# Optimization experiments

Measured on AMD Instinct MI355X. Metric: run time of the kernel, lower is better.

Reference implementation:

```python
import jax, jax.numpy as jnp
import numpy as np

B, T, C = 4, 2048, 1024


def setup_inputs() -> dict:
    key = jax.random.key(0)
    ks = jax.random.split(key, 7)
    s = 1.0 / np.sqrt(C)
    return {
        "x": jax.random.normal(ks[0], (B, T, C), dtype=jnp.float32),
        "Wq": jax.random.normal(ks[1], (C, C), dtype=jnp.float32) * s,
        "bq": jnp.zeros((C,), dtype=jnp.float32),
        "Wk": jax.random.normal(ks[2], (C, C), dtype=jnp.float32) * s,
        "bk": jnp.zeros((C,), dtype=jnp.float32),
        "Wv": jax.random.normal(ks[3], (C, C), dtype=jnp.float32) * s,
        "bv": jnp.zeros((C,), dtype=jnp.float32),
    }


def reference(x, Wq, bq, Wk, bk, Wv, bv):
    # q/k/v projections (torch Linear: x @ W^T + b; here W stored as [C_in, C_out])
    q = x @ Wq + bq  # (B, T, C)
    k = x @ Wk + bk
    v = x @ Wv + bv
    scale = 1.0 / jnp.sqrt(jnp.asarray(C, dtype=x.dtype))
    att = jnp.einsum("btc,bsc->bts", q, k) * scale  # (B, T, T)
    # causal mask: additive -inf above the diagonal
    causal = jnp.tril(jnp.ones((T, T), dtype=bool))
    att = jnp.where(causal, att, jnp.asarray(-jnp.inf, dtype=att.dtype))
    att = jax.nn.softmax(att, axis=-1)
    # dropout is identity in eval/reference mode
    out = jnp.einsum("bts,bsc->btc", att, v)  # (B, T, C)
    return out
```

## Files before the change

### kernel.cpp

```cpp
#include <hip/hip_runtime.h>

#define B_ 4
#define T_ 2048
#define C_ 1024

typedef unsigned short u16;
typedef unsigned int u32;
typedef short sh8 __attribute__((ext_vector_type(8)));
typedef float f32x4 __attribute__((ext_vector_type(4)));

__device__ __forceinline__ float bf2f(u16 u) {
    union { float f; u32 i; } c; c.i = ((u32)u) << 16; return c.f;
}
__device__ __forceinline__ u16 f2bf(float f) {
    union { float f; u32 i; } c; c.f = f;
    return (u16)((c.i + 0x7FFFu + ((c.i >> 16) & 1u)) >> 16);
}

__device__ __forceinline__ void gload_lds16(const void* g, void* l) {
    __builtin_amdgcn_global_load_lds(
        (const __attribute__((address_space(1))) u32*)g,
        (__attribute__((address_space(3))) u32*)l, 16, 0, 0);
}

template<bool RS>
__device__ __forceinline__ void mm_core(
    const u16* __restrict__ A, const u16* __restrict__ B,
    int ldA, int ldB, int nk64,
    u16* lA, u16* lB, f32x4 (&acc)[4][4], f32x4* rsacc, int tid)
{
    const int w  = tid >> 6, l = tid & 63;
    const int fr = l & 15,  fq = l >> 4;
    const int wm = (w & 1) << 6, wn = (w >> 1) << 6;
    const int rl = l >> 3;
    const int pc = l & 7;
    const int cg = pc ^ rl;

    sh8 ones;
    if (RS) {
#pragma unroll
        for (int e = 0; e < 8; ++e) ones[e] = (short)0x3F80;
    }

    for (int kt = 0; kt < nk64; ++kt) {
        const int ko = kt << 6;
#pragma unroll
        for (int t = 0; t < 4; ++t) {
            const int r0 = w * 32 + t * 8;
            const int r  = r0 + rl;
            gload_lds16(A + (size_t)r * ldA + ko + cg * 8, lA + ((size_t)r0 * 8 + l) * 8);
            gload_lds16(B + (size_t)r * ldB + ko + cg * 8, lB + ((size_t)r0 * 8 + l) * 8);
        }
        __syncthreads();
#pragma unroll
        for (int kk = 0; kk < 2; ++kk) {
            sh8 af[4], bf[4];
            const int g = kk * 4 + fq;
#pragma unroll
            for (int i = 0; i < 4; ++i) {
                const int m = wm + i * 16 + fr;
                af[i] = *(const sh8*)(lA + ((size_t)m * 8 + (g ^ (m & 7))) * 8);
                const int n = wn + i * 16 + fr;
                bf[i] = *(const sh8*)(lB + ((size_t)n * 8 + (g ^ (n & 7))) * 8);
            }
#pragma unroll
            for (int i = 0; i < 4; ++i) {
#pragma unroll
                for (int j = 0; j < 4; ++j)
                    acc[i][j] = __builtin_amdgcn_mfma_f32_16x16x32_bf16(af[i], bf[j], acc[i][j], 0, 0, 0);
                if (RS)
                    rsacc[i] = __builtin_amdgcn_mfma_f32_16x16x32_bf16(af[i], ones, rsacc[i], 0, 0, 0);
            }
        }
        __syncthreads();
    }
}

__global__ __launch_bounds__(256) void cvt_all(
    const float* __restrict__ x,
    const float* __restrict__ Wq, const float* __restrict__ Wk, const float* __restrict__ Wv,
    u16* __restrict__ xb, u16* __restrict__ wt)
{
    __shared__ float tile[64][68];
    const int bid = blockIdx.x;
    if (bid < 8192) {
        size_t i = ((size_t)bid * 256 + threadIdx.x) * 4;
        float4 f = *(const float4*)(x + i);
        ushort4 o;
        o.x = f2bf(f.x); o.y = f2bf(f.y); o.z = f2bf(f.z); o.w = f2bf(f.w);
        *(ushort4*)(xb + i) = o;
        return;
    }
    const int r = bid - 8192;
    const int z = r >> 8;
    const int rr = r & 255;
    const int n0 = (rr & 15) * 64, k0 = (rr >> 4) * 64;
    const float* W = z == 0 ? Wq : (z == 1 ? Wk : Wv);
    u16* out = wt + (size_t)z * C_ * C_;
    const int tx = threadIdx.x & 15, ty = threadIdx.x >> 4;
#pragma unroll
    for (int rr2 = 0; rr2 < 4; ++rr2) {
        int row = ty + rr2 * 16;
        *(float4*)&tile[row][tx * 4] = *(const float4*)(W + (size_t)(k0 + row) * C_ + n0 + tx * 4);
    }
    __syncthreads();
#pragma unroll
    for (int rr2 = 0; rr2 < 4; ++rr2) {
        int n = ty + rr2 * 16;
        ushort4 o;
        o.x = f2bf(tile[tx * 4 + 0][n]);
        o.y = f2bf(tile[tx * 4 + 1][n]);
        o.z = f2bf(tile[tx * 4 + 2][n]);
        o.w = f2bf(tile[tx * 4 + 3][n]);
        *(ushort4*)(out + (size_t)(n0 + n) * C_ + k0 + tx * 4) = o;
    }
}

__global__ __launch_bounds__(256, 4) void qkv_mfma(
    const u16* __restrict__ xb, const u16* __restrict__ wt,
    const float* __restrict__ bq, const float* __restrict__ bk, const float* __restrict__ bv,
    u16* __restrict__ qo, u16* __restrict__ ko, u16* __restrict__ vto)
{
    __shared__ __align__(16) u16 smem[17408];
    u16* lA = smem; u16* lB = smem + 8192;
    const int z = blockIdx.z;
    const u16* W = wt + (size_t)z * C_ * C_;
    const float* bias = z == 0 ? bq : (z == 1 ? bk : bv);
    const int n0 = blockIdx.x * 128, m0 = blockIdx.y * 128;
    const int tid = threadIdx.x;
    f32x4 acc[4][4];
#pragma unroll
    for (int i = 0; i < 4; ++i)
#pragma unroll
        for (int j = 0; j < 4; ++j) acc[i][j] = 0.0f;

    mm_core<false>(xb + (size_t)m0 * C_, W + (size_t)n0 * C_, C_, C_, C_ / 64, lA, lB, acc, nullptr, tid);

    const int w = tid >> 6, l = tid & 63, fr = l & 15, fq = l >> 4;
    const int wm = (w & 1) << 6, wn = (w >> 1) << 6;
    if (z < 2) {
#pragma unroll
        for (int i = 0; i < 4; ++i)
#pragma unroll
            for (int j = 0; j < 4; ++j) {
                const int ln = wn + j * 16 + fr;
                const float bb = bias[n0 + ln];
#pragma unroll
                for (int r = 0; r < 4; ++r) {
                    const int lm = wm + i * 16 + fq * 4 + r;
                    smem[lm * 136 + ln] = f2bf(acc[i][j][r] + bb);
                }
            }
        __syncthreads();
        u16* out = z == 0 ? qo : ko;
        const int rr = tid >> 4, cc = tid & 15;
#pragma unroll
        for (int p = 0; p < 8; ++p) {
            const int row = p * 16 + rr;
            uint4 val = *(const uint4*)&smem[row * 136 + cc * 8];
            *(uint4*)(out + (size_t)(m0 + row) * C_ + n0 + cc * 8) = val;
        }
    } else {
#pragma unroll
        for (int i = 0; i < 4; ++i)
#pragma unroll
            for (int j = 0; j < 4; ++j) {
                const int ln = wn + j * 16 + fr;
                const float bb = bias[n0 + ln];
#pragma unroll
                for (int r = 0; r < 4; ++r) {
                    const int lm = wm + i * 16 + fq * 4 + r;
                    smem[lm * 129 + ln] = f2bf(acc[i][j][r] + bb);
                }
            }
        __syncthreads();
        const int b = m0 >> 11;
        const int t0 = m0 & 2047;
        u16* vt = vto + (size_t)b * C_ * T_;
#pragma unroll
        for (int pass = 0; pass < 8; ++pass) {
            const int ln = (tid >> 4) + pass * 16;
            const int c  = tid & 15;
            u16 tmp[8];
#pragma unroll
            for (int e = 0; e < 8; ++e) tmp[e] = smem[(c * 8 + e) * 129 + ln];
            *(uint4*)(vt + (size_t)(n0 + ln) * T_ + t0 + c * 8) = *(uint4*)tmp;
        }
    }
}

__device__ __constant__ size_t att_off[4] = {
    0, (size_t)1 << 22, (size_t)1 << 25, ((size_t)1 << 25) + ((size_t)1 << 22)
};

__global__ __launch_bounds__(256, 4) void scores_mfma(
    const u16* __restrict__ qb, const u16* __restrict__ kb, u16* __restrict__ wsbase)
{
    int t = blockIdx.x;
    int by = (int)((sqrtf(8.f * t + 1.f) - 1.f) * 0.5f);
    while ((by + 1) * (by + 2) / 2 <= t) ++by;
    while (by * (by + 1) / 2 > t) --by;
    const int bx = t - by * (by + 1) / 2;
    const int b = blockIdx.z;
    const int s0 = bx * 128, m0 = by * 128;
    __shared__ __align__(16) u16 smem[17408];
    u16* lA = smem; u16* lB = smem + 8192;
    const u16* Q = qb + (size_t)b * T_ * C_ + (size_t)m0 * C_;
    const u16* K = kb + (size_t)b * T_ * C_ + (size_t)s0 * C_;
    const int tid = threadIdx.x;
    f32x4 acc[4][4];
#pragma unroll
    for (int i = 0; i < 4; ++i)
#pragma unroll
        for (int j = 0; j < 4; ++j) acc[i][j] = 0.0f;

    mm_core<false>(Q, K, C_, C_, C_ / 64, lA, lB, acc, nullptr, tid);

    const int w = tid >> 6, l = tid & 63, fr = l & 15, fq = l >> 4;
    const int wm = (w & 1) << 6, wn = (w >> 1) << 6;
#pragma unroll
    for (int i = 0; i < 4; ++i)
#pragma unroll
        for (int r = 0; r < 4; ++r) {
            const int lm = wm + i * 16 + fq * 4 + r;
            const int m = m0 + lm;
#pragma unroll
            for (int j = 0; j < 4; ++j) {
                const int ls = wn + j * 16 + fr;
                const int s = s0 + ls;
                float e = (s <= m) ? __expf(acc[i][j][r] * 0.03125f) : 0.f;
                smem[lm * 136 + ls] = f2bf(e);
            }
        }
    __syncthreads();
    u16* att = wsbase + att_off[b] + (size_t)m0 * T_ + s0;
    const int rr = tid >> 4, cc = tid & 15;
#pragma unroll
    for (int p = 0; p < 8; ++p) {
        const int row = p * 16 + rr;
        uint4 val = *(const uint4*)&smem[row * 136 + cc * 8];
        *(uint4*)(att + (size_t)row * T_ + cc * 8) = val;
    }
}

__global__ __launch_bounds__(256, 4) void pv_mfma(
    const u16* __restrict__ wsbase, const u16* __restrict__ vt,
    float* __restrict__ outp)
{
    const int b = blockIdx.z;
    const int n0 = blockIdx.x * 128;
    const int by = 15 - blockIdx.y;
    const int m0 = by * 128;
    __shared__ __align__(16) u16 smem[17408];
    u16* lA = smem; u16* lB = smem + 8192;
    const u16* A  = wsbase + att_off[b] + (size_t)m0 * T_;
    const u16* Bp = vt + (size_t)b * C_ * T_ + (size_t)n0 * T_;
    const int tid = threadIdx.x;
    f32x4 acc[4][4], rs[4];
#pragma unroll
    for (int i = 0; i < 4; ++i) {
        rs[i] = 0.0f;
#pragma unroll
        for (int j = 0; j < 4; ++j) acc[i][j] = 0.0f;
    }

    mm_core<true>(A, Bp, T_, T_, (m0 + 128) >> 6, lA, lB, acc, rs, tid);

    const int w = tid >> 6, l = tid & 63, fr = l & 15, fq = l >> 4;
    const int wm = (w & 1) << 6, wn = (w >> 1) << 6;
    float* fb = (float*)smem;
#pragma unroll
    for (int p = 0; p < 2; ++p) {
        if ((w & 1) == p) {
#pragma unroll
            for (int i = 0; i < 4; ++i)
#pragma unroll
                for (int r = 0; r < 4; ++r) {
                    const int rr2 = i * 16 + fq * 4 + r;
                    const float inv = 1.0f / rs[i][r];
#pragma unroll
                    for (int j = 0; j < 4; ++j)
                        fb[rr2 * 132 + wn + j * 16 + fr] = acc[i][j][r] * inv;
                }
        }
        __syncthreads();
        const int rr = tid >> 5, cc = (tid & 31) * 4;
#pragma unroll
        for (int k2 = 0; k2 < 8; ++k2) {
            const int row = k2 * 8 + rr;
            float4 val = *(const float4*)&fb[row * 132 + cc];
            *(float4*)(outp + ((size_t)b * T_ + m0 + p * 64 + row) * C_ + n0 + cc) = val;
        }
        __syncthreads();
    }
}

extern "C" void kernel_launch(void* const* d_in, const int* in_sizes, int n_in,
                              void* d_out, int out_size, void* d_ws, size_t ws_size,
                              hipStream_t stream) {
    const float* x  = (const float*)d_in[0];
    const float* Wq = (const float*)d_in[1];
    const float* bq = (const float*)d_in[2];
    const float* Wk = (const float*)d_in[3];
    const float* bk = (const float*)d_in[4];
    const float* Wv = (const float*)d_in[5];
    const float* bv = (const float*)d_in[6];
    float* out = (float*)d_out;

    char* ws = (char*)d_ws;
    u16* xb   = (u16*)ws;
    u16* q    = (u16*)(ws + (16ull << 20));
    u16* k    = (u16*)(ws + (32ull << 20));
    u16* vt   = (u16*)(ws + (48ull << 20));
    u16* wt   = (u16*)(ws + (64ull << 20));
    u16* attb = (u16*)ws;

    cvt_all <<<8960, 256, 0, stream>>>(x, Wq, Wk, Wv, xb, wt);
    qkv_mfma<<<dim3(8, 64, 3), 256, 0, stream>>>(xb, wt, bq, bk, bv, q, k, vt);
    scores_mfma<<<dim3(136, 1, 4), 256, 0, stream>>>(q, k, attb);
    pv_mfma    <<<dim3(8, 16, 4), 256, 0, stream>>>(attb, vt, out);
}
```

Measured before the change: 250.3 us.

## Prefetch next K-tile into registers and stage through LDS in GEMM core

Replaces direct global-to-LDS loads with register-staged prefetching: the next 64-wide K slice is loaded into registers while MFMAs run on the current LDS tile, then written to swizzled LDS at the top of the next iteration. One of the two barriers per iteration is dropped, and explicit syncs are added after each mm_core call so the epilogue can safely reuse shared memory. Launch bounds for pv_mfma are relaxed to 3 waves per SIMD to allow the extra prefetch registers. This trades register pressure and possible lower occupancy for hiding global load latency behind compute.

```diff
diff --git a/kernel.cpp b/kernel.cpp
--- a/kernel.cpp
+++ b/kernel.cpp
@@ -15,12 +15,6 @@
 __device__ __forceinline__ u16 f2bf(float f) {
     union { float f; u32 i; } c; c.f = f;
     return (u16)((c.i + 0x7FFFu + ((c.i >> 16) & 1u)) >> 16);
-}
-
-__device__ __forceinline__ void gload_lds16(const void* g, void* l) {
-    __builtin_amdgcn_global_load_lds(
-        (const __attribute__((address_space(1))) u32*)g,
-        (__attribute__((address_space(3))) u32*)l, 16, 0, 0);
 }
 
 template<bool RS>
@@ -32,9 +26,8 @@
     const int w  = tid >> 6, l = tid & 63;
     const int fr = l & 15,  fq = l >> 4;
     const int wm = (w & 1) << 6, wn = (w >> 1) << 6;
-    const int rl = l >> 3;
-    const int pc = l & 7;
-    const int cg = pc ^ rl;
+    const int sr = tid >> 3;
+    const int sc = tid & 7;
 
     sh8 ones;
     if (RS) {
@@ -42,16 +35,33 @@
         for (int e = 0; e < 8; ++e) ones[e] = (short)0x3F80;
     }
 
+    uint4 ca[4], cb[4];
+#pragma unroll
+    for (int t = 0; t < 4; ++t) {
+        const int r = sr + 32 * t;
+        ca[t] = *(const uint4*)(A + (size_t)r * ldA + sc * 8);
+        cb[t] = *(const uint4*)(B + (size_t)r * ldB + sc * 8);
+    }
+
     for (int kt = 0; kt < nk64; ++kt) {
-        const int ko = kt << 6;
+        __builtin_amdgcn_s_barrier();
 #pragma unroll
         for (int t = 0; t < 4; ++t) {
-            const int r0 = w * 32 + t * 8;
-            const int r  = r0 + rl;
-            gload_lds16(A + (size_t)r * ldA + ko + cg * 8, lA + ((size_t)r0 * 8 + l) * 8);
-            gload_lds16(B + (size_t)r * ldB + ko + cg * 8, lB + ((size_t)r0 * 8 + l) * 8);
-        }
-        __syncthreads();
+            const int r  = sr + 32 * t;
+            const int pc = sc ^ (r & 7);
+            *(uint4*)(lA + ((size_t)r * 8 + pc) * 8) = ca[t];
+            *(uint4*)(lB + ((size_t)r * 8 + pc) * 8) = cb[t];
+        }
+        __syncthreads();
+        if (kt + 1 < nk64) {
+            const int ko = (kt + 1) << 6;
+#pragma unroll
+            for (int t = 0; t < 4; ++t) {
+                const int r = sr + 32 * t;
+                ca[t] = *(const uint4*)(A + (size_t)r * ldA + ko + sc * 8);
+                cb[t] = *(const uint4*)(B + (size_t)r * ldB + ko + sc * 8);
+            }
+        }
 #pragma unroll
         for (int kk = 0; kk < 2; ++kk) {
             sh8 af[4], bf[4];
@@ -72,7 +82,6 @@
                     rsacc[i] = __builtin_amdgcn_mfma_f32_16x16x32_bf16(af[i], ones, rsacc[i], 0, 0, 0);
             }
         }
-        __syncthreads();
     }
 }
 
@@ -135,6 +144,7 @@
         for (int j = 0; j < 4; ++j) acc[i][j] = 0.0f;
 
     mm_core<false>(xb + (size_t)m0 * C_, W + (size_t)n0 * C_, C_, C_, C_ / 64, lA, lB, acc, nullptr, tid);
+    __syncthreads();
 
     const int w = tid >> 6, l = tid & 63, fr = l & 15, fq = l >> 4;
     const int wm = (w & 1) << 6, wn = (w >> 1) << 6;
@@ -215,6 +225,7 @@
         for (int j = 0; j < 4; ++j) acc[i][j] = 0.0f;
 
     mm_core<false>(Q, K, C_, C_, C_ / 64, lA, lB, acc, nullptr, tid);
+    __syncthreads();
 
     const int w = tid >> 6, l = tid & 63, fr = l & 15, fq = l >> 4;
     const int wm = (w & 1) << 6, wn = (w >> 1) << 6;
@@ -243,7 +254,7 @@
     }
 }
 
-__global__ __launch_bounds__(256, 4) void pv_mfma(
+__global__ __launch_bounds__(256, 3) void pv_mfma(
     const u16* __restrict__ wsbase, const u16* __restrict__ vt,
     float* __restrict__ outp)
 {
@@ -265,6 +276,7 @@
     }
 
     mm_core<true>(A, Bp, T_, T_, (m0 + 128) >> 6, lA, lB, acc, rs, tid);
+    __syncthreads();
 
     const int w = tid >> 6, l = tid & 63, fr = l & 15, fq = l >> 4;
     const int wm = (w & 1) << 6, wn = (w >> 1) << 6;
```

New measurement: 693.6 us. +177.2%, slower.

## Double-buffer LDS tiles in shared MFMA GEMM core with async prefetch

Applied to the files above, without the earlier changes.

The shared GEMM mainloop now keeps two LDS buffers and issues the global-to-LDS loads for tile k+2 while tile k is computed. It waits with explicit vmcnt counts and raw barriers instead of __syncthreads around every tile. LDS per block doubles to 64 KB and launch bounds drop to 2 blocks per CU, so global memory latency should be hidden by prefetch rather than by occupancy. The raw waitcnt and barrier sequencing needs correct counts, or the LDS reads can race with in-flight loads.

```diff
diff --git a/kernel.cpp b/kernel.cpp
--- a/kernel.cpp
+++ b/kernel.cpp
@@ -23,11 +23,15 @@
         (__attribute__((address_space(3))) u32*)l, 16, 0, 0);
 }
 
+__device__ __forceinline__ void wait_vm8()   { asm volatile("s_waitcnt vmcnt(8)" ::: "memory"); }
+__device__ __forceinline__ void wait_vm0()   { asm volatile("s_waitcnt vmcnt(0)" ::: "memory"); }
+__device__ __forceinline__ void barrier_raw(){ asm volatile("s_barrier" ::: "memory"); }
+
 template<bool RS>
 __device__ __forceinline__ void mm_core(
     const u16* __restrict__ A, const u16* __restrict__ B,
     int ldA, int ldB, int nk64,
-    u16* lA, u16* lB, f32x4 (&acc)[4][4], f32x4* rsacc, int tid)
+    u16* lds, f32x4 (&acc)[4][4], f32x4* rsacc, int tid)
 {
     const int w  = tid >> 6, l = tid & 63;
     const int fr = l & 15,  fq = l >> 4;
@@ -42,16 +46,27 @@
         for (int e = 0; e < 8; ++e) ones[e] = (short)0x3F80;
     }
 
-    for (int kt = 0; kt < nk64; ++kt) {
+    auto issue = [&](int kt) {
         const int ko = kt << 6;
+        u16* dA = lds + ((kt & 1) << 14);
+        u16* dB = dA + 8192;
 #pragma unroll
         for (int t = 0; t < 4; ++t) {
             const int r0 = w * 32 + t * 8;
             const int r  = r0 + rl;
-            gload_lds16(A + (size_t)r * ldA + ko + cg * 8, lA + ((size_t)r0 * 8 + l) * 8);
-            gload_lds16(B + (size_t)r * ldB + ko + cg * 8, lB + ((size_t)r0 * 8 + l) * 8);
-        }
-        __syncthreads();
+            gload_lds16(A + (size_t)r * ldA + ko + cg * 8, dA + ((size_t)r0 * 8 + l) * 8);
+            gload_lds16(B + (size_t)r * ldB + ko + cg * 8, dB + ((size_t)r0 * 8 + l) * 8);
+        }
+    };
+
+    issue(0);
+    issue(1);
+
+    for (int kt = 0; kt < nk64; ++kt) {
+        if (kt + 1 < nk64) wait_vm8(); else wait_vm0();
+        barrier_raw();
+        u16* bufA = lds + ((kt & 1) << 14);
+        u16* bufB = bufA + 8192;
 #pragma unroll
         for (int kk = 0; kk < 2; ++kk) {
             sh8 af[4], bf[4];
@@ -59,9 +74,9 @@
 #pragma unroll
             for (int i = 0; i < 4; ++i) {
                 const int m = wm + i * 16 + fr;
-                af[i] = *(const sh8*)(lA + ((size_t)m * 8 + (g ^ (m & 7))) * 8);
+                af[i] = *(const sh8*)(bufA + ((size_t)m * 8 + (g ^ (m & 7))) * 8);
                 const int n = wn + i * 16 + fr;
-                bf[i] = *(const sh8*)(lB + ((size_t)n * 8 + (g ^ (n & 7))) * 8);
+                bf[i] = *(const sh8*)(bufB + ((size_t)n * 8 + (g ^ (n & 7))) * 8);
             }
 #pragma unroll
             for (int i = 0; i < 4; ++i) {
@@ -72,7 +87,8 @@
                     rsacc[i] = __builtin_amdgcn_mfma_f32_16x16x32_bf16(af[i], ones, rsacc[i], 0, 0, 0);
             }
         }
-        __syncthreads();
+        barrier_raw();
+        if (kt + 2 < nk64) issue(kt + 2);
     }
 }
 
@@ -116,13 +132,12 @@
     }
 }
 
-__global__ __launch_bounds__(256, 4) void qkv_mfma(
+__global__ __launch_bounds__(256, 2) void qkv_mfma(
     const u16* __restrict__ xb, const u16* __restrict__ wt,
     const float* __restrict__ bq, const float* __restrict__ bk, const float* __restrict__ bv,
     u16* __restrict__ qo, u16* __restrict__ ko, u16* __restrict__ vto)
 {
-    __shared__ __align__(16) u16 smem[17408];
-    u16* lA = smem; u16* lB = smem + 8192;
+    __shared__ __align__(16) u16 smem[32768];
     const int z = blockIdx.z;
     const u16* W = wt + (size_t)z * C_ * C_;
     const float* bias = z == 0 ? bq : (z == 1 ? bk : bv);
@@ -134,7 +149,7 @@
 #pragma unroll
         for (int j = 0; j < 4; ++j) acc[i][j] = 0.0f;
 
-    mm_core<false>(xb + (size_t)m0 * C_, W + (size_t)n0 * C_, C_, C_, C_ / 64, lA, lB, acc, nullptr, tid);
+    mm_core<false>(xb + (size_t)m0 * C_, W + (size_t)n0 * C_, C_, C_, C_ / 64, smem, acc, nullptr, tid);
 
     const int w = tid >> 6, l = tid & 63, fr = l & 15, fq = l >> 4;
     const int wm = (w & 1) << 6, wn = (w >> 1) << 6;
@@ -193,7 +208,7 @@
     0, (size_t)1 << 22, (size_t)1 << 25, ((size_t)1 << 25) + ((size_t)1 << 22)
 };
 
-__global__ __launch_bounds__(256, 4) void scores_mfma(
+__global__ __launch_bounds__(256, 2) void scores_mfma(
     const u16* __restrict__ qb, const u16* __restrict__ kb, u16* __restrict__ wsbase)
 {
     int t = blockIdx.x;
@@ -203,8 +218,7 @@
     const int bx = t - by * (by + 1) / 2;
     const int b = blockIdx.z;
     const int s0 = bx * 128, m0 = by * 128;
-    __shared__ __align__(16) u16 smem[17408];
-    u16* lA = smem; u16* lB = smem + 8192;
+    __shared__ __align__(16) u16 smem[32768];
     const u16* Q = qb + (size_t)b * T_ * C_ + (size_t)m0 * C_;
     const u16* K = kb + (size_t)b * T_ * C_ + (size_t)s0 * C_;
     const int tid = threadIdx.x;
@@ -214,7 +228,7 @@
 #pragma unroll
         for (int j = 0; j < 4; ++j) acc[i][j] = 0.0f;
 
-    mm_core<false>(Q, K, C_, C_, C_ / 64, lA, lB, acc, nullptr, tid);
+    mm_core<false>(Q, K, C_, C_, C_ / 64, smem, acc, nullptr, tid);
 
     const int w = tid >> 6, l = tid & 63, fr = l & 15, fq = l >> 4;
     const int wm = (w & 1) << 6, wn = (w >> 1) << 6;
@@ -243,7 +257,7 @@
     }
 }
 
-__global__ __launch_bounds__(256, 4) void pv_mfma(
+__global__ __launch_bounds__(256, 2) void pv_mfma(
     const u16* __restrict__ wsbase, const u16* __restrict__ vt,
     float* __restrict__ outp)
 {
@@ -251,8 +265,7 @@
     const int n0 = blockIdx.x * 128;
     const int by = 15 - blockIdx.y;
     const int m0 = by * 128;
-    __shared__ __align__(16) u16 smem[17408];
-    u16* lA = smem; u16* lB = smem + 8192;
+    __shared__ __align__(16) u16 smem[32768];
     const u16* A  = wsbase + att_off[b] + (size_t)m0 * T_;
     const u16* Bp = vt + (size_t)b * C_ * T_ + (size_t)n0 * T_;
     const int tid = threadIdx.x;
@@ -264,7 +277,7 @@
         for (int j = 0; j < 4; ++j) acc[i][j] = 0.0f;
     }
 
-    mm_core<true>(A, Bp, T_, T_, (m0 + 128) >> 6, lA, lB, acc, rs, tid);
+    mm_core<true>(A, Bp, T_, T_, (m0 + 128) >> 6, smem, acc, rs, tid);
 
     const int w = tid >> 6, l = tid & 63, fr = l & 15, fq = l >> 4;
     const int wm = (w & 1) << 6, wn = (w >> 1) << 6;
```

Result: no change. 246.6 us (-1.5%).
